# Kernel tuning notes

Measured on AMD Instinct MI355X. Metric: run time of the kernel, lower is better.

The kernel has to match this reference:

```python
import jax, jax.numpy as jnp
import numpy as np

CAMS, HEADS, PTS, LAYERS = 6, 8, 2, 3
D, DH, FFN = 256, 32, 512
VZ, VH, VW = 8, 50, 50
NQ = VZ * VH * VW
IN_C = 768
IMG_H, IMG_W = 256, 704
FH, FW = IMG_H // 32, IMG_W // 32   # 8, 22
L = FH * FW                         # 176 tokens per camera
LVIS = 44                           # visible tokens (mask_ratio=0.75)


def _layer_norm(x, g, b, eps=1e-5):
    m = x.mean(-1, keepdims=True)
    v = x.var(-1, keepdims=True)
    return (x - m) / jnp.sqrt(v + eps) * g + b


def _group_norm(x, g, b, groups=16, eps=1e-5):
    B, C = x.shape[0], x.shape[1]
    xg = x.reshape(B, groups, C // groups, *x.shape[2:])
    m = xg.mean(axis=(2, 3, 4, 5), keepdims=True)
    v = xg.var(axis=(2, 3, 4, 5), keepdims=True)
    xg = (xg - m) / jnp.sqrt(v + eps)
    return xg.reshape(x.shape) * g[None, :, None, None, None] + b[None, :, None, None, None]


def _bilinear(val, loc, Hf, Wf):
    # val: [C, HW, heads, dh]; loc: [C, NQ, heads, P, 2] as (x, y) pixel coords
    x, y = loc[..., 0], loc[..., 1]
    x0 = jnp.floor(x); y0 = jnp.floor(y)
    wx, wy = x - x0, y - y0
    x0i, y0i = x0.astype(jnp.int32), y0.astype(jnp.int32)
    cidx = jnp.arange(val.shape[0])[:, None, None, None]
    hidx = jnp.arange(val.shape[2])[None, None, :, None]

    def g(yi, xi):
        idx = jnp.clip(yi, 0, Hf - 1) * Wf + jnp.clip(xi, 0, Wf - 1)
        return val[cidx, idx, hidx]  # [C,NQ,heads,P,dh]

    out = ((1 - wx) * (1 - wy))[..., None] * g(y0i, x0i)
    out = out + (wx * (1 - wy))[..., None] * g(y0i, x0i + 1)
    out = out + ((1 - wx) * wy)[..., None] * g(y0i + 1, x0i)
    out = out + (wx * wy)[..., None] * g(y0i + 1, x0i + 1)
    return out


def setup_inputs() -> dict:
    key = jax.random.key(0)
    ks = iter(jax.random.split(key, 48))

    def rn(shape, s=0.02):
        return jax.random.normal(next(ks), shape, jnp.float32) * s

    return {
        'camera_x': jax.random.normal(next(ks), (CAMS, LVIS, IN_C), jnp.float32),
        'camera_ids_restore': jax.random.randint(next(ks), (CAMS, L), 0, L),
        'img_h': IMG_H, 'img_w': IMG_W,
        'mask_token': rn((1, 1, IN_C)),
        'vol_emb': rn((NQ, D), 1.0),
        'W_tc': rn((D, IN_C)), 'b_tc': jnp.zeros((D,), jnp.float32),
        'cams_embeds': rn((CAMS, D), 1.0),
        'level_embeds': rn((1, D), 1.0),
        'W_off': rn((LAYERS, D, HEADS * CAMS * PTS * 2)),
        'b_off': rn((LAYERS, HEADS * CAMS * PTS * 2), 2.0),
        'W_att': rn((LAYERS, D, HEADS * CAMS * PTS)),
        'b_att': jnp.zeros((LAYERS, HEADS * CAMS * PTS), jnp.float32),
        'W_val': rn((LAYERS, D, D)), 'b_val': jnp.zeros((LAYERS, D), jnp.float32),
        'W_out': rn((LAYERS, D, D)), 'b_out': jnp.zeros((LAYERS, D), jnp.float32),
        'ln1_g': jnp.ones((LAYERS, D), jnp.float32), 'ln1_b': jnp.zeros((LAYERS, D), jnp.float32),
        'W_ff1': rn((LAYERS, D, FFN)), 'b_ff1': jnp.zeros((LAYERS, FFN), jnp.float32),
        'W_ff2': rn((LAYERS, FFN, D)), 'b_ff2': jnp.zeros((LAYERS, D), jnp.float32),
        'ln2_g': jnp.ones((LAYERS, D), jnp.float32), 'ln2_b': jnp.zeros((LAYERS, D), jnp.float32),
        'deconv_w': rn((D, D, 2, 2, 2)),
        'gn1_g': jnp.ones((D,), jnp.float32), 'gn1_b': jnp.zeros((D,), jnp.float32),
        'conv3_w': rn((192, D, 3, 3, 3)),
        'gn2_g': jnp.ones((192,), jnp.float32), 'gn2_b': jnp.zeros((192,), jnp.float32),
    }


def _forward(camera_x, camera_ids_restore, img_h, img_w, mask_token, vol_emb, W_tc, b_tc,
             cams_embeds, level_embeds, W_off, b_off, W_att, b_att, W_val, b_val, W_out, b_out,
             ln1_g, ln1_b, W_ff1, b_ff1, W_ff2, b_ff2, ln2_g, ln2_b,
             deconv_w, gn1_g, gn1_b, conv3_w, gn2_g, gn2_b):
    N, Lfull = camera_ids_restore.shape
    # 1) MAE unshuffle: append mask tokens, gather back to original order
    mt = jnp.broadcast_to(mask_token, (N, Lfull - camera_x.shape[1], IN_C)).astype(camera_x.dtype)
    full = jnp.concatenate([camera_x, mt], axis=1)                         # [N,L,C]
    full = jnp.take_along_axis(full, camera_ids_restore[:, :, None], axis=1)
    Hf, Wf = img_h // 32, img_w // 32
    cam_x = jnp.transpose(full, (0, 2, 1)).reshape(1, N, IN_C, Hf, Wf)     # [1,6,768,8,22]
    # 2) 1x1 transfer conv + ReLU
    vf = jax.nn.relu(jnp.einsum('bnchw,oc->bnohw', cam_x, W_tc) + b_tc[None, None, :, None, None])
    # 3) flatten spatial + cam/level embeds -> per-camera feature maps [N,HW,D]
    vf = jnp.transpose(vf.reshape(1, N, D, Hf * Wf), (1, 0, 3, 2))          # [N,1,HW,D]
    vf = vf + cams_embeds[:, None, None, :] + level_embeds[None, None, 0:1, :]
    feat = vf[:, 0]                                                         # [N,HW,D]
    # 4) reference points of volume queries (z slow, h, w fast) -> pixel coords
    ww = (jnp.arange(VW, dtype=jnp.float32) + 0.5) / VW
    hh = (jnp.arange(VH, dtype=jnp.float32) + 0.5) / VH
    grid = jnp.stack([jnp.tile(ww, VH), jnp.repeat(hh, VW)], axis=-1)       # [VH*VW,2]
    ref_pix = jnp.tile(grid, (VZ, 1)) * jnp.array([Wf, Hf], jnp.float32) - 0.5  # [NQ,2]
    # 5) deformable cross-attention volume encoder
    q = vol_emb
    for l in range(LAYERS):
        off = (q @ W_off[l] + b_off[l]).reshape(NQ, HEADS, CAMS, PTS, 2)
        att = jax.nn.softmax((q @ W_att[l] + b_att[l]).reshape(NQ, HEADS, CAMS * PTS), axis=-1)
        att = jnp.transpose(att.reshape(NQ, HEADS, CAMS, PTS), (2, 0, 1, 3))      # [C,NQ,H,P]
        val = (feat @ W_val[l] + b_val[l]).reshape(CAMS, Hf * Wf, HEADS, DH)
        loc = jnp.transpose(ref_pix[:, None, None, None, :] + off, (2, 0, 1, 3, 4))  # [C,NQ,H,P,2]
        sampled = _bilinear(val, loc, Hf, Wf)                                     # [C,NQ,H,P,DH]
        agg = jnp.einsum('cnhp,cnhpd->nhd', att, sampled).reshape(NQ, D)
        q = _layer_norm(q + agg @ W_out[l] + b_out[l], ln1_g[l], ln1_b[l])
        q = _layer_norm(q + jax.nn.relu(q @ W_ff1[l] + b_ff1[l]) @ W_ff2[l] + b_ff2[l], ln2_g[l], ln2_b[l])
    # 6) reshape -> [1, D, VW, VH, VZ] (matches .permute(0,4,3,2,1))
    vol = jnp.transpose(q.reshape(1, VZ, VH, VW, D), (0, 4, 3, 2, 1))
    # 7) deblock: deconv3d(k=2,s=2) -> GN16 -> ReLU -> conv3d(k=3,p=1) -> GN16 -> ReLU
    x = jax.lax.conv_transpose(vol, deconv_w, (2, 2, 2), 'VALID',
                               dimension_numbers=('NCDHW', 'OIDHW', 'NCDHW'))
    x = jax.nn.relu(_group_norm(x, gn1_g, gn1_b))
    x = jax.lax.conv_general_dilated(x, conv3_w, (1, 1, 1), [(1, 1)] * 3,
                                     dimension_numbers=('NCDHW', 'OIDHW', 'NCDHW'))
    x = jax.nn.relu(_group_norm(x, gn2_g, gn2_b))
    return x, cam_x


def reference(camera_x, camera_ids_restore, img_h, img_w, mask_token, vol_emb, W_tc, b_tc,
              cams_embeds, level_embeds, W_off, b_off, W_att, b_att, W_val, b_val, W_out, b_out,
              ln1_g, ln1_b, W_ff1, b_ff1, W_ff2, b_ff2, ln2_g, ln2_b,
              deconv_w, gn1_g, gn1_b, conv3_w, gn2_g, gn2_b):
    return _forward(camera_x, camera_ids_restore, img_h, img_w, mask_token, vol_emb, W_tc, b_tc,
                    cams_embeds, level_embeds, W_off, b_off, W_att, b_att, W_val, b_val, W_out, b_out,
                    ln1_g, ln1_b, W_ff1, b_ff1, W_ff2, b_ff2, ln2_g, ln2_b,
                    deconv_w, gn1_g, gn1_b, conv3_w, gn2_g, gn2_b)
```

## Files before the change

### kernel.cpp

```cpp
#include <hip/hip_runtime.h>
#include <stdint.h>

typedef __attribute__((ext_vector_type(8))) short s16x8;
typedef __attribute__((ext_vector_type(4))) float f32x4;

static __device__ __forceinline__ unsigned short f2bf(float f) {
  unsigned u = __float_as_uint(f);
  u += 0x7FFFu + ((u >> 16) & 1u);
  return (unsigned short)(u >> 16);
}
static __device__ __forceinline__ float bf2f(unsigned short h) {
  return __uint_as_float(((unsigned)h) << 16);
}

__global__ void k_wt(const float* __restrict__ in, unsigned short* __restrict__ out,
                     int K, int N, int outL, int total) {
  int idx = blockIdx.x * 256 + threadIdx.x;
  if (idx >= total) return;
  int kn = K * N;
  int l = idx / kn, r = idx - l * kn;
  int k = r / N, n = r - k * N;
  out[(size_t)l * outL + (size_t)n * K + k] = f2bf(in[idx]);
}

__global__ void k_wdc(const float* __restrict__ in, unsigned short* __restrict__ out) {
  int idx = blockIdx.x * 256 + threadIdx.x;
  int n = idx >> 8, k = idx & 255;
  out[idx] = f2bf(in[((size_t)(n & 255)) * 2048 + k * 8 + (n >> 8)]);
}

__global__ void k_wc3(const float* __restrict__ W, unsigned short* __restrict__ T) {
  int idx = blockIdx.x * 256 + threadIdx.x;
  int tap = idx / 49152;
  int rem = idx - tap * 49152;
  int oc = rem >> 8, ic = rem & 255;
  T[idx] = f2bf(W[(oc * 256 + ic) * 27 + tap]);
}

__global__ void k_cvt(const float* __restrict__ in, unsigned short* __restrict__ out, int n) {
  int i = blockIdx.x * 256 + threadIdx.x;
  if (i < n) out[i] = f2bf(in[i]);
}

__global__ void k_wtct(const float* __restrict__ W, float* __restrict__ T) {
  int idx = blockIdx.x * 256 + threadIdx.x;
  int k = idx >> 8, o = idx & 255;
  T[idx] = W[o * 768 + k];
}

__global__ void k_restore(const float* __restrict__ cx, const int* __restrict__ ids,
                          const float* __restrict__ mtok, float* __restrict__ out) {
  int idx = blockIdx.x * 256 + threadIdx.x;
  int p = idx % 176;
  int r = idx / 176;
  int ch = r % 768;
  int c = r / 768;
  int id = ids[c * 176 + p];
  out[idx] = (id < 44) ? cx[((size_t)(c * 44 + id)) * 768 + ch] : mtok[ch];
}

__global__ __launch_bounds__(256) void k_vf(const float* __restrict__ camx, const float* __restrict__ WtT,
                                            const float* __restrict__ btc, const float* __restrict__ cemb,
                                            const float* __restrict__ lemb, unsigned short* __restrict__ featb) {
  __shared__ float sa[768];
  int blk = blockIdx.x;
  int c = blk / 176, p = blk - c * 176;
  int t = threadIdx.x;
  for (int i = t; i < 768; i += 256) sa[i] = camx[((size_t)(c * 768 + i)) * 176 + p];
  __syncthreads();
  float acc = 0.f;
  for (int k = 0; k < 768; ++k) acc += sa[k] * WtT[k * 256 + t];
  featb[(size_t)blk * 256 + t] = f2bf(fmaxf(acc + btc[t], 0.f) + cemb[c * 256 + t] + lemb[t]);
}

__global__ __launch_bounds__(256) void k_gemm(
    const unsigned short* __restrict__ A, int M, int lda,
    const unsigned short* __restrict__ Bt, int K, int N,
    const float* __restrict__ bias, const float* __restrict__ bias2, int n1, int relu,
    float* __restrict__ Cf, unsigned short* __restrict__ Cb, int ldc, int mode) {
  __shared__ short sA[128 * 40];
  const int t = threadIdx.x;
  const int l = t & 63, w = t >> 6;
  const int lo = l & 15, kg = l >> 4;
  const int row0 = blockIdx.x * 128, n0 = blockIdx.y * 64;
  const s16x8 bz = {0, 0, 0, 0, 0, 0, 0, 0};
  f32x4 acc[2][4] = {};
  s16x8 bc[4], bn[4];
#pragma unroll
  for (int nb = 0; nb < 4; ++nb) {
    int n = n0 + nb * 16 + lo;
    bc[nb] = (n < N) ? *(const s16x8*)&Bt[(size_t)n * K + kg * 8] : bz;
  }
  const int stR = t >> 1, stH = t & 1;
  for (int kc = 0; kc < K; kc += 32) {
    const bool pf = (kc + 32 < K);
    if (pf) {
#pragma unroll
      for (int nb = 0; nb < 4; ++nb) {
        int n = n0 + nb * 16 + lo;
        bn[nb] = (n < N) ? *(const s16x8*)&Bt[(size_t)n * K + kc + 32 + kg * 8] : bz;
      }
    }
    __syncthreads();
    {
      int r = row0 + stR;
      uint4 v0 = {0u, 0u, 0u, 0u}, v1 = {0u, 0u, 0u, 0u};
      if (r < M) {
        const unsigned short* src = A + (size_t)r * lda + kc + stH * 16;
        v0 = *(const uint4*)src;
        v1 = *(const uint4*)(src + 8);
      }
      *(uint4*)&sA[stR * 40 + stH * 16] = v0;
      *(uint4*)&sA[stR * 40 + stH * 16 + 8] = v1;
    }
    __syncthreads();
    s16x8 a0 = *(const s16x8*)&sA[(w * 32 + lo) * 40 + kg * 8];
    s16x8 a1 = *(const s16x8*)&sA[(w * 32 + 16 + lo) * 40 + kg * 8];
#pragma unroll
    for (int nb = 0; nb < 4; ++nb) {
      acc[0][nb] = __builtin_amdgcn_mfma_f32_16x16x32_bf16(a0, bc[nb], acc[0][nb], 0, 0, 0);
      acc[1][nb] = __builtin_amdgcn_mfma_f32_16x16x32_bf16(a1, bc[nb], acc[1][nb], 0, 0, 0);
    }
    if (pf) {
#pragma unroll
      for (int nb = 0; nb < 4; ++nb) bc[nb] = bn[nb];
    }
  }
#pragma unroll
  for (int m = 0; m < 2; ++m)
#pragma unroll
    for (int nb = 0; nb < 4; ++nb)
#pragma unroll
      for (int r = 0; r < 4; ++r) {
        int row = row0 + w * 32 + m * 16 + (kg << 2) + r;
        int col = n0 + nb * 16 + lo;
        if (row < M && col < N) {
          float v = acc[m][nb][r];
          if (bias) v += (col < n1) ? bias[col] : bias2[col - n1];
          if (relu) v = fmaxf(v, 0.f);
          if (mode == 0) {
            Cf[(size_t)row * ldc + col] = v;
          } else if (mode == 2) {
            Cb[(size_t)row * ldc + col] = f2bf(v);
          } else {
            int tap = col >> 8, oc = col & 255;
            int z = row / 2500, rr = row - z * 2500;
            int hy = rr / 50, wx = rr - hy * 50;
            int t1 = tap >> 2, t2 = (tap >> 1) & 1, t3 = tap & 1;
            int od = 2 * wx + 1 - t1, oh = 2 * hy + 1 - t2, ow = 2 * z + 1 - t3;
            Cb[((size_t)((od * 100 + oh) * 16 + ow)) * 256 + oc] = f2bf(v);
          }
        }
      }
}

__global__ __launch_bounds__(256) void k_sample(const float* __restrict__ oa,
                                                const float* __restrict__ val,
                                                unsigned short* __restrict__ aggb) {
  __shared__ float sl[96], sw[96];
  int n = blockIdx.x, t = threadIdx.x;
  if (t < 96) sl[t] = oa[(size_t)n * 288 + 192 + t];
  __syncthreads();
  if (t < 8) {
    float mx = -1e30f;
    for (int j = 0; j < 12; ++j) mx = fmaxf(mx, sl[t * 12 + j]);
    float s = 0.f;
    for (int j = 0; j < 12; ++j) s += __expf(sl[t * 12 + j] - mx);
    float inv = 1.f / s;
    for (int j = 0; j < 12; ++j) sw[t * 12 + j] = __expf(sl[t * 12 + j] - mx) * inv;
  }
  __syncthreads();
  int h = t >> 5, d = t & 31;
  float xr = ((float)(n % 50) + 0.5f) * (22.0f / 50.0f) - 0.5f;
  float yr = ((float)((n / 50) % 50) + 0.5f) * (8.0f / 50.0f) - 0.5f;
  float acc = 0.f;
  const float* offn = oa + (size_t)n * 288 + h * 24;
  const float* vbh = val + (size_t)h * 32 + d;
#pragma unroll
  for (int c = 0; c < 6; ++c)
#pragma unroll
    for (int p2 = 0; p2 < 2; ++p2) {
      float x = xr + offn[(c * 2 + p2) * 2];
      float y = yr + offn[(c * 2 + p2) * 2 + 1];
      float x0 = floorf(x), y0 = floorf(y);
      float wx = x - x0, wy = y - y0;
      int ix0 = min(max((int)x0, 0), 21), ix1 = min(max((int)x0 + 1, 0), 21);
      int iy0 = min(max((int)y0, 0), 7), iy1 = min(max((int)y0 + 1, 0), 7);
      const float* vb = vbh + (size_t)c * 176 * 256;
      float v00 = vb[(size_t)(iy0 * 22 + ix0) * 256];
      float v01 = vb[(size_t)(iy0 * 22 + ix1) * 256];
      float v10 = vb[(size_t)(iy1 * 22 + ix0) * 256];
      float v11 = vb[(size_t)(iy1 * 22 + ix1) * 256];
      float bil = (1.f - wx) * (1.f - wy) * v00 + wx * (1.f - wy) * v01 +
                  (1.f - wx) * wy * v10 + wx * wy * v11;
      acc += sw[h * 12 + c * 2 + p2] * bil;
    }
  aggb[(size_t)n * 256 + t] = f2bf(acc);
}

__global__ __launch_bounds__(256) void k_addln(float* __restrict__ q, const float* __restrict__ p,
                                               const float* __restrict__ g, const float* __restrict__ b,
                                               unsigned short* __restrict__ qb) {
  __shared__ float red[8];
  int n = blockIdx.x, t = threadIdx.x;
  float x = q[(size_t)n * 256 + t] + p[(size_t)n * 256 + t];
  float s1 = x, s2 = x * x;
#pragma unroll
  for (int o = 32; o >= 1; o >>= 1) {
    s1 += __shfl_xor(s1, o, 64);
    s2 += __shfl_xor(s2, o, 64);
  }
  int w = t >> 6;
  if ((t & 63) == 0) { red[w * 2] = s1; red[w * 2 + 1] = s2; }
  __syncthreads();
  s1 = red[0] + red[2] + red[4] + red[6];
  s2 = red[1] + red[3] + red[5] + red[7];
  float mean = s1 * (1.0f / 256.0f);
  float var = s2 * (1.0f / 256.0f) - mean * mean;
  float y = (x - mean) * rsqrtf(var + 1e-5f) * g[t] + b[t];
  q[(size_t)n * 256 + t] = y;
  qb[(size_t)n * 256 + t] = f2bf(y);
}

__global__ __launch_bounds__(256) void k_gnstat1(const unsigned short* __restrict__ X, float* __restrict__ part) {
  __shared__ float s1[256], s2[256];
  int b = blockIdx.x, t = threadIdx.x;
  unsigned base = (unsigned)b * 16384u + (unsigned)t;
  float a = 0.f, q = 0.f;
  for (int i = 0; i < 64; ++i) { float v = bf2f(X[base + (unsigned)i * 256u]); a += v; q += v * v; }
  s1[t] = a; s2[t] = q;
  __syncthreads();
  for (int s = 8; s > 0; s >>= 1) {
    if ((t & 15) < s) { s1[t] += s1[t + s]; s2[t] += s2[t + s]; }
    __syncthreads();
  }
  if ((t & 15) == 0) {
    part[(t >> 4) * 2500 + b] = s1[t];
    part[40000 + (t >> 4) * 2500 + b] = s2[t];
  }
}

__global__ __launch_bounds__(256) void k_gnred1(const float* __restrict__ part, float* __restrict__ gmv) {
  __shared__ float s1[256], s2[256];
  int g = blockIdx.x, t = threadIdx.x;
  float a = 0.f, q = 0.f;
  for (int i = t; i < 2500; i += 256) { a += part[g * 2500 + i]; q += part[40000 + g * 2500 + i]; }
  s1[t] = a; s2[t] = q;
  __syncthreads();
  for (int s = 128; s > 0; s >>= 1) {
    if (t < s) { s1[t] += s1[t + s]; s2[t] += s2[t + s]; }
    __syncthreads();
  }
  if (t == 0) {
    float m = s1[0] / 2560000.0f;
    float v = s2[0] / 2560000.0f - m * m;
    gmv[2 * g] = m; gmv[2 * g + 1] = rsqrtf(v + 1e-5f);
  }
}

__global__ __launch_bounds__(256) void k_gnapply1(unsigned short* __restrict__ X, const float* __restrict__ gmv,
                                                  const float* __restrict__ g, const float* __restrict__ b) {
  for (unsigned idx = blockIdx.x * 256 + threadIdx.x; idx < 40960000u; idx += gridDim.x * 256) {
    int oc = idx & 255, grp = oc >> 4;
    float v = bf2f(X[idx]);
    v = (v - gmv[grp * 2]) * gmv[grp * 2 + 1] * g[oc] + b[oc];
    X[idx] = f2bf(fmaxf(v, 0.f));
  }
}

__global__ __launch_bounds__(256, 2) void k_conv3(const unsigned short* __restrict__ X,
                                                  const unsigned short* __restrict__ Wp,
                                                  unsigned short* __restrict__ Y) {
  __shared__ short sX[4 * 543 * 8];
  __shared__ short sW[2][768 * 8];
  int bid = blockIdx.x;
  int xcd = bid & 7, idx = bid >> 3;
  int swz = (xcd < 4 ? xcd * 163 : 652 + (xcd - 4) * 162) + idx;
  const int od = swz / 13;
  const int oh0 = (swz - od * 13) * 8;
  const int t = threadIdx.x;
  const int l = t & 63, w = t >> 6;
  const int kg = l >> 4, lo = l & 15;
  f32x4 acc[8][3] = {};
  const int oc0 = t >> 2, oc1 = (t + 256) >> 2, oc2 = (t + 512) >> 2;
  const int kgs = t & 3;
  const int g0 = 4 * oc0 + (kgs ^ (oc0 & 3));
  const int g1 = 4 * oc1 + (kgs ^ (oc1 & 3));
  const int g2 = 4 * oc2 + (kgs ^ (oc2 & 3));
  int woff[3];
#pragma unroll
  for (int nb = 0; nb < 3; ++nb)
    woff[nb] = (4 * (w * 48 + nb * 16 + lo) + (kg ^ (lo & 3))) * 8;

  int cur = 0;
  for (int chunk = 0; chunk < 8; ++chunk) {
#pragma unroll
    for (int i = 0; i < 9; ++i) {
      int e = t + i * 256;
      if (e < 2160) {
        int pos = e >> 2, ks = e & 3;
        int sd = pos / 180, r2 = pos - sd * 180;
        int sh = r2 / 18, sw_ = r2 - sh * 18;
        int gd = od + sd - 1, gh = oh0 + sh - 1, gw = sw_ - 1;
        uint4 v = {0u, 0u, 0u, 0u};
        if ((unsigned)gd < 100u && (unsigned)gh < 100u && (unsigned)gw < 16u)
          v = *(const uint4*)&X[((size_t)((gd * 100 + gh) * 16 + gw)) * 256 + chunk * 32 + ks * 8];
        *(uint4*)&sX[(ks * 543 + pos) * 8] = v;
      }
    }
    if (chunk == 0) {
      *(uint4*)&sW[0][g0 * 8] = *(const uint4*)&Wp[(size_t)oc0 * 256 + kgs * 8];
      *(uint4*)&sW[0][g1 * 8] = *(const uint4*)&Wp[(size_t)oc1 * 256 + kgs * 8];
      *(uint4*)&sW[0][g2 * 8] = *(const uint4*)&Wp[(size_t)oc2 * 256 + kgs * 8];
    }
    __syncthreads();
    for (int tap = 0; tap < 27; ++tap) {
      int ntap = tap + 1, nch = chunk;
      if (ntap == 27) { ntap = 0; ++nch; }
      const bool pf = (nch < 8);
      uint4 wr0, wr1, wr2;
      if (pf) {
        const unsigned short* wb = Wp + (size_t)ntap * 49152 + nch * 32 + kgs * 8;
        wr0 = *(const uint4*)&wb[(size_t)oc0 * 256];
        wr1 = *(const uint4*)&wb[(size_t)oc1 * 256];
        wr2 = *(const uint4*)&wb[(size_t)oc2 * 256];
      }
      const int t1 = tap / 9, tr = tap - t1 * 9, t2 = tr / 3, t3 = tr - t2 * 3;
      const short* swc = sW[cur];
      s16x8 b0 = *(const s16x8*)&swc[woff[0]];
      s16x8 b1 = *(const s16x8*)&swc[woff[1]];
      s16x8 b2 = *(const s16x8*)&swc[woff[2]];
#pragma unroll
      for (int m = 0; m < 8; ++m) {
        int pos = t1 * 180 + (m + t2) * 18 + lo + t3;
        s16x8 a = *(const s16x8*)&sX[(kg * 543 + pos) * 8];
        acc[m][0] = __builtin_amdgcn_mfma_f32_16x16x32_bf16(a, b0, acc[m][0], 0, 0, 0);
        acc[m][1] = __builtin_amdgcn_mfma_f32_16x16x32_bf16(a, b1, acc[m][1], 0, 0, 0);
        acc[m][2] = __builtin_amdgcn_mfma_f32_16x16x32_bf16(a, b2, acc[m][2], 0, 0, 0);
      }
      if (pf) {
        short* swn = sW[cur ^ 1];
        *(uint4*)&swn[g0 * 8] = wr0;
        *(uint4*)&swn[g1 * 8] = wr1;
        *(uint4*)&swn[g2 * 8] = wr2;
      }
      cur ^= 1;
      __syncthreads();
    }
  }
#pragma unroll
  for (int m = 0; m < 8; ++m) {
    int oh = oh0 + m;
    if (oh < 100) {
#pragma unroll
      for (int nb = 0; nb < 3; ++nb)
#pragma unroll
        for (int r = 0; r < 4; ++r) {
          int oc = w * 48 + nb * 16 + lo;
          int ow = (kg << 2) + r;
          Y[(size_t)oc * 160000 + (size_t)((od * 100 + oh) * 16) + ow] = f2bf(acc[m][nb][r]);
        }
    }
  }
}

__global__ __launch_bounds__(256) void k_gnstat2(const unsigned short* __restrict__ X, float* __restrict__ part) {
  __shared__ float s1[256], s2[256];
  int b = blockIdx.x, t = threadIdx.x;
  int ch = b / 10, pp = b - ch * 10;
  unsigned base = (unsigned)ch * 160000u + (unsigned)pp * 16000u;
  float a = 0.f, q = 0.f;
  for (int i = t; i < 16000; i += 256) { float v = bf2f(X[base + i]); a += v; q += v * v; }
  s1[t] = a; s2[t] = q;
  __syncthreads();
  for (int s = 128; s > 0; s >>= 1) {
    if (t < s) { s1[t] += s1[t + s]; s2[t] += s2[t + s]; }
    __syncthreads();
  }
  if (t == 0) { part[80000 + ch * 10 + pp] = s1[0]; part[81920 + ch * 10 + pp] = s2[0]; }
}

__global__ __launch_bounds__(256) void k_gnred2(const float* __restrict__ part, float* __restrict__ gmv) {
  __shared__ float s1[256], s2[256];
  int g = blockIdx.x, t = threadIdx.x;
  float a = (t < 120) ? part[80000 + g * 120 + t] : 0.f;
  float q = (t < 120) ? part[81920 + g * 120 + t] : 0.f;
  s1[t] = a; s2[t] = q;
  __syncthreads();
  for (int s = 128; s > 0; s >>= 1) {
    if (t < s) { s1[t] += s1[t + s]; s2[t] += s2[t + s]; }
    __syncthreads();
  }
  if (t == 0) {
    float m = s1[0] / 1920000.0f;
    float v = s2[0] / 1920000.0f - m * m;
    gmv[2 * g] = m; gmv[2 * g + 1] = rsqrtf(v + 1e-5f);
  }
}

__global__ __launch_bounds__(256) void k_gnapply2(const unsigned short* __restrict__ X, const float* __restrict__ gmv,
                                                  const float* __restrict__ g, const float* __restrict__ b,
                                                  float* __restrict__ out) {
  for (unsigned idx = blockIdx.x * 256 + threadIdx.x; idx < 30720000u; idx += gridDim.x * 256) {
    unsigned oc = idx / 160000u;
    unsigned grp = oc / 12u;
    float v = bf2f(X[idx]);
    v = (v - gmv[grp * 2]) * gmv[grp * 2 + 1] * g[oc] + b[oc];
    out[idx] = fmaxf(v, 0.f);
  }
}

static inline dim3 gemm_grid(int M, int N) { return dim3((M + 127) / 128, (N + 63) / 64); }

extern "C" void kernel_launch(void* const* d_in, const int* in_sizes, int n_in,
                              void* d_out, int out_size, void* d_ws, size_t ws_size,
                              hipStream_t stream) {
  const float* camera_x = (const float*)d_in[0];
  const int* ids = (const int*)d_in[1];
  const float* mask_tok = (const float*)d_in[4];
  const float* vol_emb = (const float*)d_in[5];
  const float* W_tc = (const float*)d_in[6];
  const float* b_tc = (const float*)d_in[7];
  const float* cams_emb = (const float*)d_in[8];
  const float* lvl_emb = (const float*)d_in[9];
  const float* W_off = (const float*)d_in[10];
  const float* b_off = (const float*)d_in[11];
  const float* W_att = (const float*)d_in[12];
  const float* b_att = (const float*)d_in[13];
  const float* W_val = (const float*)d_in[14];
  const float* b_val = (const float*)d_in[15];
  const float* W_out = (const float*)d_in[16];
  const float* b_out = (const float*)d_in[17];
  const float* ln1_g = (const float*)d_in[18];
  const float* ln1_b = (const float*)d_in[19];
  const float* W_ff1 = (const float*)d_in[20];
  const float* b_ff1 = (const float*)d_in[21];
  const float* W_ff2 = (const float*)d_in[22];
  const float* b_ff2 = (const float*)d_in[23];
  const float* ln2_g = (const float*)d_in[24];
  const float* ln2_b = (const float*)d_in[25];
  const float* deconv_w = (const float*)d_in[26];
  const float* gn1_g = (const float*)d_in[27];
  const float* gn1_b = (const float*)d_in[28];
  const float* conv3_w = (const float*)d_in[29];
  const float* gn2_g = (const float*)d_in[30];
  const float* gn2_b = (const float*)d_in[31];

  char* ws = (char*)d_ws;
  float* q             = (float*)(ws + 0);
  unsigned short* qb   = (unsigned short*)(ws + 20480000);
  float* proj          = (float*)(ws + 30720000);
  float* oa            = (float*)(ws + 51200000);
  unsigned short* aggb = (unsigned short*)(ws + 74240000);
  unsigned short* ffhb = (unsigned short*)(ws + 84480000);
  float* val           = (float*)(ws + 104960000);
  unsigned short* featb= (unsigned short*)(ws + 106041344);
  unsigned short* x1bf = (unsigned short*)(ws + 30720000);
  unsigned short* c3   = (unsigned short*)(ws + 112640000);
  unsigned short* Wt_val = (unsigned short*)(ws + 174080000);
  unsigned short* Wt_oa  = (unsigned short*)(ws + 174473216);
  unsigned short* Wt_out = (unsigned short*)(ws + 174915584);
  unsigned short* Wt_ff1 = (unsigned short*)(ws + 175308800);
  unsigned short* Wt_ff2 = (unsigned short*)(ws + 176095232);
  unsigned short* Wt_dc  = (unsigned short*)(ws + 176881664);
  unsigned short* wc3    = (unsigned short*)(ws + 177930240);
  float* part = (float*)(ws + 180584448);
  float* gmv1 = (float*)(ws + 180920320);
  float* gmv2 = (float*)(ws + 180920448);
  float* wtcT = (float*)(ws + 180920576);

  float* out_x = (float*)d_out;
  float* out_camx = out_x + 30720000;

  k_wtct<<<768, 256, 0, stream>>>(W_tc, wtcT);
  k_wt<<<(3 * 65536 + 255) / 256, 256, 0, stream>>>(W_val, Wt_val, 256, 256, 65536, 3 * 65536);
  k_wt<<<(3 * 49152 + 255) / 256, 256, 0, stream>>>(W_off, Wt_oa, 256, 192, 73728, 3 * 49152);
  k_wt<<<(3 * 24576 + 255) / 256, 256, 0, stream>>>(W_att, Wt_oa + 192 * 256, 256, 96, 73728, 3 * 24576);
  k_wt<<<(3 * 65536 + 255) / 256, 256, 0, stream>>>(W_out, Wt_out, 256, 256, 65536, 3 * 65536);
  k_wt<<<(3 * 131072 + 255) / 256, 256, 0, stream>>>(W_ff1, Wt_ff1, 256, 512, 131072, 3 * 131072);
  k_wt<<<(3 * 131072 + 255) / 256, 256, 0, stream>>>(W_ff2, Wt_ff2, 512, 256, 131072, 3 * 131072);
  k_wdc<<<2048, 256, 0, stream>>>(deconv_w, Wt_dc);
  k_wc3<<<5184, 256, 0, stream>>>(conv3_w, wc3);

  k_restore<<<3168, 256, 0, stream>>>(camera_x, ids, mask_tok, out_camx);
  k_vf<<<1056, 256, 0, stream>>>(out_camx, wtcT, b_tc, cams_emb, lvl_emb, featb);
  hipMemcpyAsync(q, vol_emb, (size_t)20000 * 256 * 4, hipMemcpyDeviceToDevice, stream);
  k_cvt<<<20000, 256, 0, stream>>>(vol_emb, qb, 5120000);

  for (int lyr = 0; lyr < 3; ++lyr) {
    k_gemm<<<gemm_grid(1056, 256), 256, 0, stream>>>(featb, 1056, 256, Wt_val + lyr * 65536, 256, 256,
                                                     b_val + lyr * 256, nullptr, 256, 0, val, nullptr, 256, 0);
    k_gemm<<<gemm_grid(20000, 288), 256, 0, stream>>>(qb, 20000, 256, Wt_oa + lyr * 73728, 256, 288,
                                                      b_off + lyr * 192, b_att + lyr * 96, 192, 0,
                                                      oa, nullptr, 288, 0);
    k_sample<<<20000, 256, 0, stream>>>(oa, val, aggb);
    k_gemm<<<gemm_grid(20000, 256), 256, 0, stream>>>(aggb, 20000, 256, Wt_out + lyr * 65536, 256, 256,
                                                      b_out + lyr * 256, nullptr, 256, 0, proj, nullptr, 256, 0);
    k_addln<<<20000, 256, 0, stream>>>(q, proj, ln1_g + lyr * 256, ln1_b + lyr * 256, qb);
    k_gemm<<<gemm_grid(20000, 512), 256, 0, stream>>>(qb, 20000, 256, Wt_ff1 + lyr * 131072, 256, 512,
                                                      b_ff1 + lyr * 512, nullptr, 512, 1, nullptr, ffhb, 512, 2);
    k_gemm<<<gemm_grid(20000, 256), 256, 0, stream>>>(ffhb, 20000, 512, Wt_ff2 + lyr * 131072, 512, 256,
                                                      b_ff2 + lyr * 256, nullptr, 256, 0, proj, nullptr, 256, 0);
    k_addln<<<20000, 256, 0, stream>>>(q, proj, ln2_g + lyr * 256, ln2_b + lyr * 256, qb);
  }

  k_gemm<<<gemm_grid(20000, 2048), 256, 0, stream>>>(qb, 20000, 256, Wt_dc, 256, 2048,
                                                     nullptr, nullptr, 2048, 0, nullptr, x1bf, 256, 1);

  k_gnstat1<<<2500, 256, 0, stream>>>(x1bf, part);
  k_gnred1<<<16, 256, 0, stream>>>(part, gmv1);
  k_gnapply1<<<2048, 256, 0, stream>>>(x1bf, gmv1, gn1_g, gn1_b);

  k_conv3<<<1300, 256, 0, stream>>>(x1bf, wc3, c3);

  k_gnstat2<<<1920, 256, 0, stream>>>(c3, part);
  k_gnred2<<<16, 256, 0, stream>>>(part, gmv2);
  k_gnapply2<<<2048, 256, 0, stream>>>(c3, gmv2, gn2_g, gn2_b, out_x);
}
```

Measured before the change: 1.512 ms.

## Restructure conv3d weight path into register fragments and vectorize GroupNorm kernels

The conv3d weight tensor is pre-permuted into MFMA fragment order, so each lane loads its B operands straight from global memory into registers. This removes the LDS weight double buffer and the per-tap barriers. The conv loop now groups taps by their (t1,t3) offset, so each A fragment loaded from LDS is reused across three t2 taps. Separately, the GroupNorm stat and apply kernels now use 16-byte vector loads and stores on bf16 data. The cost is higher register pressure from 18 prefetched weight fragments and reliance on global/L2 bandwidth for weights.

```diff
diff --git a/kernel.cpp b/kernel.cpp
--- a/kernel.cpp
+++ b/kernel.cpp
@@ -11,6 +11,16 @@
 }
 static __device__ __forceinline__ float bf2f(unsigned short h) {
   return __uint_as_float(((unsigned)h) << 16);
+}
+static __device__ __forceinline__ void sum8(uint4 u, float& a, float& q) {
+  unsigned w[4] = {u.x, u.y, u.z, u.w};
+#pragma unroll
+  for (int i = 0; i < 4; ++i) {
+    float v0 = __uint_as_float((w[i] & 0xFFFFu) << 16);
+    float v1 = __uint_as_float(w[i] & 0xFFFF0000u);
+    a += v0 + v1;
+    q += v0 * v0 + v1 * v1;
+  }
 }
 
 __global__ void k_wt(const float* __restrict__ in, unsigned short* __restrict__ out,
@@ -34,7 +44,10 @@
   int tap = idx / 49152;
   int rem = idx - tap * 49152;
   int oc = rem >> 8, ic = rem & 255;
-  T[idx] = f2bf(W[(oc * 256 + ic) * 27 + tap]);
+  int chunk = ic >> 5, kg = (ic >> 3) & 3, j = ic & 7;
+  int ocblk = oc >> 4, lo = oc & 15;
+  size_t frag = (size_t)(tap * 8 + chunk) * 12 + ocblk;
+  T[(frag * 64 + kg * 16 + lo) * 8 + j] = f2bf(W[(oc * 256 + ic) * 27 + tap]);
 }
 
 __global__ void k_cvt(const float* __restrict__ in, unsigned short* __restrict__ out, int n) {
@@ -225,18 +238,25 @@
 __global__ __launch_bounds__(256) void k_gnstat1(const unsigned short* __restrict__ X, float* __restrict__ part) {
   __shared__ float s1[256], s2[256];
   int b = blockIdx.x, t = threadIdx.x;
-  unsigned base = (unsigned)b * 16384u + (unsigned)t;
+  int oc8 = t & 31, v0 = t >> 5;
   float a = 0.f, q = 0.f;
-  for (int i = 0; i < 64; ++i) { float v = bf2f(X[base + (unsigned)i * 256u]); a += v; q += v * v; }
+#pragma unroll
+  for (int i = 0; i < 8; ++i) {
+    int vox = v0 + i * 8;
+    uint4 u = *(const uint4*)&X[(size_t)b * 16384 + vox * 256 + oc8 * 8];
+    sum8(u, a, q);
+  }
   s1[t] = a; s2[t] = q;
   __syncthreads();
-  for (int s = 8; s > 0; s >>= 1) {
-    if ((t & 15) < s) { s1[t] += s1[t + s]; s2[t] += s2[t + s]; }
-    __syncthreads();
-  }
-  if ((t & 15) == 0) {
-    part[(t >> 4) * 2500 + b] = s1[t];
-    part[40000 + (t >> 4) * 2500 + b] = s2[t];
+  if (t < 128) { s1[t] += s1[t + 128]; s2[t] += s2[t + 128]; }
+  __syncthreads();
+  if (t < 64) { s1[t] += s1[t + 64]; s2[t] += s2[t + 64]; }
+  __syncthreads();
+  if (t < 32) { s1[t] += s1[t + 32]; s2[t] += s2[t + 32]; }
+  __syncthreads();
+  if (t < 16) {
+    part[t * 2500 + b] = s1[2 * t] + s1[2 * t + 1];
+    part[40000 + t * 2500 + b] = s2[2 * t] + s2[2 * t + 1];
   }
 }
 
@@ -260,11 +280,26 @@
 
 __global__ __launch_bounds__(256) void k_gnapply1(unsigned short* __restrict__ X, const float* __restrict__ gmv,
                                                   const float* __restrict__ g, const float* __restrict__ b) {
-  for (unsigned idx = blockIdx.x * 256 + threadIdx.x; idx < 40960000u; idx += gridDim.x * 256) {
-    int oc = idx & 255, grp = oc >> 4;
-    float v = bf2f(X[idx]);
-    v = (v - gmv[grp * 2]) * gmv[grp * 2 + 1] * g[oc] + b[oc];
-    X[idx] = f2bf(fmaxf(v, 0.f));
+  for (unsigned i = blockIdx.x * 256 + threadIdx.x; i < 5120000u; i += gridDim.x * 256) {
+    unsigned e = i * 8u;
+    int oc0 = e & 255, grp = oc0 >> 4;
+    float mean = gmv[grp * 2], rstd = gmv[grp * 2 + 1];
+    float4 g0 = *(const float4*)&g[oc0], g1 = *(const float4*)&g[oc0 + 4];
+    float4 b0 = *(const float4*)&b[oc0], b1 = *(const float4*)&b[oc0 + 4];
+    uint4 u = *(const uint4*)&X[e];
+    unsigned w[4] = {u.x, u.y, u.z, u.w};
+    float gg[8] = {g0.x, g0.y, g0.z, g0.w, g1.x, g1.y, g1.z, g1.w};
+    float bb[8] = {b0.x, b0.y, b0.z, b0.w, b1.x, b1.y, b1.z, b1.w};
+    unsigned o[4];
+#pragma unroll
+    for (int j = 0; j < 4; ++j) {
+      float v0 = __uint_as_float((w[j] & 0xFFFFu) << 16);
+      float v1 = __uint_as_float(w[j] & 0xFFFF0000u);
+      v0 = fmaxf((v0 - mean) * rstd * gg[2 * j] + bb[2 * j], 0.f);
+      v1 = fmaxf((v1 - mean) * rstd * gg[2 * j + 1] + bb[2 * j + 1], 0.f);
+      o[j] = (unsigned)f2bf(v0) | ((unsigned)f2bf(v1) << 16);
+    }
+    *(uint4*)&X[e] = make_uint4(o[0], o[1], o[2], o[3]);
   }
 }
 
@@ -272,7 +307,6 @@
                                                   const unsigned short* __restrict__ Wp,
                                                   unsigned short* __restrict__ Y) {
   __shared__ short sX[4 * 543 * 8];
-  __shared__ short sW[2][768 * 8];
   int bid = blockIdx.x;
   int xcd = bid & 7, idx = bid >> 3;
   int swz = (xcd < 4 ? xcd * 163 : 652 + (xcd - 4) * 162) + idx;
@@ -282,71 +316,64 @@
   const int l = t & 63, w = t >> 6;
   const int kg = l >> 4, lo = l & 15;
   f32x4 acc[8][3] = {};
-  const int oc0 = t >> 2, oc1 = (t + 256) >> 2, oc2 = (t + 512) >> 2;
-  const int kgs = t & 3;
-  const int g0 = 4 * oc0 + (kgs ^ (oc0 & 3));
-  const int g1 = 4 * oc1 + (kgs ^ (oc1 & 3));
-  const int g2 = 4 * oc2 + (kgs ^ (oc2 & 3));
-  int woff[3];
-#pragma unroll
-  for (int nb = 0; nb < 3; ++nb)
-    woff[nb] = (4 * (w * 48 + nb * 16 + lo) + (kg ^ (lo & 3))) * 8;
-
-  int cur = 0;
-  for (int chunk = 0; chunk < 8; ++chunk) {
-#pragma unroll
-    for (int i = 0; i < 9; ++i) {
-      int e = t + i * 256;
-      if (e < 2160) {
-        int pos = e >> 2, ks = e & 3;
-        int sd = pos / 180, r2 = pos - sd * 180;
-        int sh = r2 / 18, sw_ = r2 - sh * 18;
-        int gd = od + sd - 1, gh = oh0 + sh - 1, gw = sw_ - 1;
-        uint4 v = {0u, 0u, 0u, 0u};
-        if ((unsigned)gd < 100u && (unsigned)gh < 100u && (unsigned)gw < 16u)
-          v = *(const uint4*)&X[((size_t)((gd * 100 + gh) * 16 + gw)) * 256 + chunk * 32 + ks * 8];
-        *(uint4*)&sX[(ks * 543 + pos) * 8] = v;
+  s16x8 bc[9], bn[9];
+  const unsigned short* Wl = Wp + (size_t)l * 8;
+  const int w3 = w * 3;
+#pragma unroll
+  for (int t2 = 0; t2 < 3; ++t2)
+#pragma unroll
+    for (int nb = 0; nb < 3; ++nb)
+      bc[t2 * 3 + nb] = *(const s16x8*)&Wl[(size_t)((t2 * 3 * 8) * 12 + w3 + nb) * 512];
+
+  for (int g = 0; g < 72; ++g) {
+    const int chunk = g / 9;
+    const int sub = g - chunk * 9;
+    const int t1 = sub / 3, t3 = sub - t1 * 3;
+    if (sub == 0) {
+      __syncthreads();
+#pragma unroll
+      for (int i = 0; i < 9; ++i) {
+        int e = t + i * 256;
+        if (e < 2160) {
+          int pos = e >> 2, ks = e & 3;
+          int sd = pos / 180, r2 = pos - sd * 180;
+          int sh = r2 / 18, sw_ = r2 - sh * 18;
+          int gd = od + sd - 1, gh = oh0 + sh - 1, gw = sw_ - 1;
+          uint4 v = {0u, 0u, 0u, 0u};
+          if ((unsigned)gd < 100u && (unsigned)gh < 100u && (unsigned)gw < 16u)
+            v = *(const uint4*)&X[((size_t)((gd * 100 + gh) * 16 + gw)) * 256 + chunk * 32 + ks * 8];
+          *(uint4*)&sX[(ks * 543 + pos) * 8] = v;
+        }
       }
-    }
-    if (chunk == 0) {
-      *(uint4*)&sW[0][g0 * 8] = *(const uint4*)&Wp[(size_t)oc0 * 256 + kgs * 8];
-      *(uint4*)&sW[0][g1 * 8] = *(const uint4*)&Wp[(size_t)oc1 * 256 + kgs * 8];
-      *(uint4*)&sW[0][g2 * 8] = *(const uint4*)&Wp[(size_t)oc2 * 256 + kgs * 8];
-    }
-    __syncthreads();
-    for (int tap = 0; tap < 27; ++tap) {
-      int ntap = tap + 1, nch = chunk;
-      if (ntap == 27) { ntap = 0; ++nch; }
-      const bool pf = (nch < 8);
-      uint4 wr0, wr1, wr2;
-      if (pf) {
-        const unsigned short* wb = Wp + (size_t)ntap * 49152 + nch * 32 + kgs * 8;
-        wr0 = *(const uint4*)&wb[(size_t)oc0 * 256];
-        wr1 = *(const uint4*)&wb[(size_t)oc1 * 256];
-        wr2 = *(const uint4*)&wb[(size_t)oc2 * 256];
+      __syncthreads();
+    }
+    const int g1 = g + 1;
+    if (g1 < 72) {
+      const int c1 = g1 / 9, s1 = g1 - c1 * 9;
+      const int t1n = s1 / 3, t3n = s1 - t1n * 3;
+#pragma unroll
+      for (int t2 = 0; t2 < 3; ++t2)
+#pragma unroll
+        for (int nb = 0; nb < 3; ++nb)
+          bn[t2 * 3 + nb] = *(const s16x8*)&Wl[
+              (size_t)(((t1n * 9 + t2 * 3 + t3n) * 8 + c1) * 12 + w3 + nb) * 512];
+    }
+    const int abase = kg * 543 + t1 * 180 + lo + t3;
+#pragma unroll
+    for (int sh = 0; sh < 10; ++sh) {
+      s16x8 a = *(const s16x8*)&sX[(abase + sh * 18) * 8];
+#pragma unroll
+      for (int t2 = 0; t2 < 3; ++t2) {
+        const int m = sh - t2;
+        if (m >= 0 && m < 8) {
+          acc[m][0] = __builtin_amdgcn_mfma_f32_16x16x32_bf16(a, bc[t2 * 3 + 0], acc[m][0], 0, 0, 0);
+          acc[m][1] = __builtin_amdgcn_mfma_f32_16x16x32_bf16(a, bc[t2 * 3 + 1], acc[m][1], 0, 0, 0);
+          acc[m][2] = __builtin_amdgcn_mfma_f32_16x16x32_bf16(a, bc[t2 * 3 + 2], acc[m][2], 0, 0, 0);
+        }
       }
-      const int t1 = tap / 9, tr = tap - t1 * 9, t2 = tr / 3, t3 = tr - t2 * 3;
-      const short* swc = sW[cur];
-      s16x8 b0 = *(const s16x8*)&swc[woff[0]];
-      s16x8 b1 = *(const s16x8*)&swc[woff[1]];
-      s16x8 b2 = *(const s16x8*)&swc[woff[2]];
-#pragma unroll
-      for (int m = 0; m < 8; ++m) {
-        int pos = t1 * 180 + (m + t2) * 18 + lo + t3;
-        s16x8 a = *(const s16x8*)&sX[(kg * 543 + pos) * 8];
-        acc[m][0] = __builtin_amdgcn_mfma_f32_16x16x32_bf16(a, b0, acc[m][0], 0, 0, 0);
-        acc[m][1] = __builtin_amdgcn_mfma_f32_16x16x32_bf16(a, b1, acc[m][1], 0, 0, 0);
-        acc[m][2] = __builtin_amdgcn_mfma_f32_16x16x32_bf16(a, b2, acc[m][2], 0, 0, 0);
-      }
-      if (pf) {
-        short* swn = sW[cur ^ 1];
-        *(uint4*)&swn[g0 * 8] = wr0;
-        *(uint4*)&swn[g1 * 8] = wr1;
-        *(uint4*)&swn[g2 * 8] = wr2;
-      }
-      cur ^= 1;
-      __syncthreads();
-    }
+    }
+#pragma unroll
+    for (int i = 0; i < 9; ++i) bc[i] = bn[i];
   }
 #pragma unroll
   for (int m = 0; m < 8; ++m) {
@@ -368,9 +395,12 @@
   __shared__ float s1[256], s2[256];
   int b = blockIdx.x, t = threadIdx.x;
   int ch = b / 10, pp = b - ch * 10;
-  unsigned base = (unsigned)ch * 160000u + (unsigned)pp * 16000u;
+  const unsigned short* base = X + (size_t)ch * 160000 + (size_t)pp * 16000;
   float a = 0.f, q = 0.f;
-  for (int i = t; i < 16000; i += 256) { float v = bf2f(X[base + i]); a += v; q += v * v; }
+  for (int i = t; i < 2000; i += 256) {
+    uint4 u = *(const uint4*)&base[i * 8];
+    sum8(u, a, q);
+  }
   s1[t] = a; s2[t] = q;
   __syncthreads();
   for (int s = 128; s > 0; s >>= 1) {
@@ -401,12 +431,24 @@
 __global__ __launch_bounds__(256) void k_gnapply2(const unsigned short* __restrict__ X, const float* __restrict__ gmv,
                                                   const float* __restrict__ g, const float* __restrict__ b,
                                                   float* __restrict__ out) {
-  for (unsigned idx = blockIdx.x * 256 + threadIdx.x; idx < 30720000u; idx += gridDim.x * 256) {
-    unsigned oc = idx / 160000u;
+  for (unsigned i = blockIdx.x * 256 + threadIdx.x; i < 3840000u; i += gridDim.x * 256) {
+    unsigned oc = i / 20000u;
     unsigned grp = oc / 12u;
-    float v = bf2f(X[idx]);
-    v = (v - gmv[grp * 2]) * gmv[grp * 2 + 1] * g[oc] + b[oc];
-    out[idx] = fmaxf(v, 0.f);
+    float mean = gmv[grp * 2], rstd = gmv[grp * 2 + 1];
+    float gam = g[oc], bet = b[oc];
+    unsigned e = i * 8u;
+    uint4 u = *(const uint4*)&X[e];
+    unsigned wv[4] = {u.x, u.y, u.z, u.w};
+    float o[8];
+#pragma unroll
+    for (int j = 0; j < 4; ++j) {
+      float v0 = __uint_as_float((wv[j] & 0xFFFFu) << 16);
+      float v1 = __uint_as_float(wv[j] & 0xFFFF0000u);
+      o[2 * j] = fmaxf((v0 - mean) * rstd * gam + bet, 0.f);
+      o[2 * j + 1] = fmaxf((v1 - mean) * rstd * gam + bet, 0.f);
+    }
+    *(float4*)&out[e] = make_float4(o[0], o[1], o[2], o[3]);
+    *(float4*)&out[e + 4] = make_float4(o[4], o[5], o[6], o[7]);
   }
 }
 
```

New measurement: 1.353 ms. -10.5%, faster.
